# Kernel optimization log

Hardware: AMD Instinct MI355X
Metric: run time of the kernel (lower is better)

## Reference

```python
import jax, jax.numpy as jnp
import numpy as np

VOCAB = 100000
EMBED = 128
BATCH = 65536
NEG = 5


def setup_inputs() -> dict:
    key = jax.random.key(0)
    k1, k2, k3, k4, k5 = jax.random.split(key, 5)
    pos_w = jax.random.randint(k1, (BATCH,), 0, VOCAB)
    pos_v = jax.random.randint(k2, (BATCH,), 0, VOCAB)
    neg_v = jax.random.randint(k3, (BATCH, NEG), 0, VOCAB)
    w_table = jax.random.normal(k4, (VOCAB, EMBED), dtype=jnp.float32) * 0.01
    v_table = jax.random.normal(k5, (VOCAB, EMBED), dtype=jnp.float32) * 0.01
    return {"pos_w": pos_w, "pos_v": pos_v, "neg_v": neg_v,
            "w_table": w_table, "v_table": v_table}


def reference(pos_w, pos_v, neg_v, w_table, v_table):
    # Gathers: [B, E] and [B, K, E]
    w_emb = w_table[pos_w]          # [B, E]
    pos_v_emb = v_table[pos_v]      # [B, E]
    neg_v_emb = v_table[neg_v]      # [B, K, E]

    # Positive score: elementwise dot per row
    score1 = jnp.sum(w_emb * pos_v_emb, axis=1)          # [B]
    score1 = jnp.clip(score1, -10.0, 10.0)
    score1 = jax.nn.log_sigmoid(score1)

    # Negative scores: bmm([B,K,E], [B,E,1]) -> [B,K]
    score2 = jnp.einsum('bke,be->bk', neg_v_emb, w_emb)  # [B, K]
    score2 = jnp.clip(score2, -10.0, 10.0)
    score2 = jax.nn.log_sigmoid(-score2)

    loss = -(jnp.sum(score1) + jnp.sum(score2))
    return loss
```

## Files before the change

kernel.cpp:

```cpp
#include <hip/hip_runtime.h>

#define EMBED 128
#define NEG 5
#define ROWS_PER_BLOCK 16

__device__ __forceinline__ float dot8(float4 w0, float4 w1, float4 a0, float4 a1) {
    float s = w0.x * a0.x;
    s = fmaf(w0.y, a0.y, s);
    s = fmaf(w0.z, a0.z, s);
    s = fmaf(w0.w, a0.w, s);
    s = fmaf(w1.x, a1.x, s);
    s = fmaf(w1.y, a1.y, s);
    s = fmaf(w1.z, a1.z, s);
    s = fmaf(w1.w, a1.w, s);
    return s;
}

__global__ __launch_bounds__(256) void sgneg_kernel(
    const int* __restrict__ pos_w,
    const int* __restrict__ pos_v,
    const int* __restrict__ neg_v,
    const float* __restrict__ w_table,
    const float* __restrict__ v_table,
    float* __restrict__ out,
    int batch)
{
    const int tid = threadIdx.x;
    const int lane16 = tid & 15;
    const int row = tid >> 4;
    const int b = blockIdx.x * ROWS_PER_BLOCK + row;

    __shared__ float scores[6 * ROWS_PER_BLOCK];
    __shared__ float wsum[4];

    float d0 = 0.f, d1 = 0.f, d2 = 0.f, d3 = 0.f, d4 = 0.f, d5 = 0.f;

    if (b < batch) {
        const int iw  = pos_w[b];
        const int ipv = pos_v[b];
        const int in0 = neg_v[b * NEG + 0];
        const int in1 = neg_v[b * NEG + 1];
        const int in2 = neg_v[b * NEG + 2];
        const int in3 = neg_v[b * NEG + 3];
        const int in4 = neg_v[b * NEG + 4];

        const size_t o0 = (size_t)lane16 * 4;
        const size_t o1 = 64 + (size_t)lane16 * 4;

        const float* wr = w_table + (size_t)iw * EMBED;
        const float4 w0 = *reinterpret_cast<const float4*>(wr + o0);
        const float4 w1 = *reinterpret_cast<const float4*>(wr + o1);

        const float* pr = v_table + (size_t)ipv * EMBED;
        const float* r0 = v_table + (size_t)in0 * EMBED;
        const float* r1 = v_table + (size_t)in1 * EMBED;
        const float* r2 = v_table + (size_t)in2 * EMBED;
        const float* r3 = v_table + (size_t)in3 * EMBED;
        const float* r4 = v_table + (size_t)in4 * EMBED;

        const float4 p0 = *reinterpret_cast<const float4*>(pr + o0);
        const float4 p1 = *reinterpret_cast<const float4*>(pr + o1);
        const float4 a0 = *reinterpret_cast<const float4*>(r0 + o0);
        const float4 a1 = *reinterpret_cast<const float4*>(r0 + o1);
        const float4 b0 = *reinterpret_cast<const float4*>(r1 + o0);
        const float4 b1 = *reinterpret_cast<const float4*>(r1 + o1);
        const float4 c0 = *reinterpret_cast<const float4*>(r2 + o0);
        const float4 c1 = *reinterpret_cast<const float4*>(r2 + o1);
        const float4 e0 = *reinterpret_cast<const float4*>(r3 + o0);
        const float4 e1 = *reinterpret_cast<const float4*>(r3 + o1);
        const float4 f0 = *reinterpret_cast<const float4*>(r4 + o0);
        const float4 f1 = *reinterpret_cast<const float4*>(r4 + o1);

        d0 = dot8(w0, w1, p0, p1);
        d1 = dot8(w0, w1, a0, a1);
        d2 = dot8(w0, w1, b0, b1);
        d3 = dot8(w0, w1, c0, c1);
        d4 = dot8(w0, w1, e0, e1);
        d5 = dot8(w0, w1, f0, f1);
    }

    #pragma unroll
    for (int m = 8; m >= 1; m >>= 1) {
        d0 += __shfl_xor(d0, m, 64);
        d1 += __shfl_xor(d1, m, 64);
        d2 += __shfl_xor(d2, m, 64);
        d3 += __shfl_xor(d3, m, 64);
        d4 += __shfl_xor(d4, m, 64);
        d5 += __shfl_xor(d5, m, 64);
    }

    if (lane16 == 0) {
        scores[0 * ROWS_PER_BLOCK + row] = d0;
        scores[1 * ROWS_PER_BLOCK + row] = d1;
        scores[2 * ROWS_PER_BLOCK + row] = d2;
        scores[3 * ROWS_PER_BLOCK + row] = d3;
        scores[4 * ROWS_PER_BLOCK + row] = d4;
        scores[5 * ROWS_PER_BLOCK + row] = d5;
    }
    __syncthreads();

    float t = 0.0f;
    if (tid < 6 * ROWS_PER_BLOCK) {
        const int k = tid >> 4;
        const int r = tid & 15;
        const int gb = blockIdx.x * ROWS_PER_BLOCK + r;
        if (gb < batch) {
            float s = scores[tid];
            s = fminf(10.0f, fmaxf(-10.0f, s));
            const float arg = (k == 0) ? -s : s;
            t = __logf(1.0f + __expf(arg));
        }
    }

    #pragma unroll
    for (int m = 32; m >= 1; m >>= 1) t += __shfl_xor(t, m, 64);
    if ((tid & 63) == 0) wsum[tid >> 6] = t;
    __syncthreads();
    if (tid == 0) atomicAdd(out, wsum[0] + wsum[1] + wsum[2] + wsum[3]);
}

extern "C" void kernel_launch(void* const* d_in, const int* in_sizes, int n_in,
                              void* d_out, int out_size, void* d_ws, size_t ws_size,
                              hipStream_t stream) {
    const int*   pos_w   = (const int*)d_in[0];
    const int*   pos_v   = (const int*)d_in[1];
    const int*   neg_v   = (const int*)d_in[2];
    const float* w_table = (const float*)d_in[3];
    const float* v_table = (const float*)d_in[4];
    float* out = (float*)d_out;

    const int batch = in_sizes[0];

    hipMemsetAsync(out, 0, sizeof(float), stream);

    const int blocks = (batch + ROWS_PER_BLOCK - 1) / ROWS_PER_BLOCK;
    sgneg_kernel<<<blocks, 256, 0, stream>>>(pos_w, pos_v, neg_v,
                                             w_table, v_table, out, batch);
}
```

Measured before the change: 167.1 us.

## Process four rows per 16-lane group to raise memory-level parallelism

Each 16-lane group now handles four batch rows, so a block covers 64 rows. All index loads and 56 float4 gathers are issued before any compute, which raises the number of outstanding memory requests per thread. It also cuts the block count and the number of atomics by a factor of four. The cost is much higher register pressure, which the launch_bounds hint of 4 caps, and out-of-range rows are clamped to the last row instead of skipped.

Result: faster. 141.4 us (-15.4%).

```diff
diff --git a/kernel.cpp b/kernel.cpp
--- a/kernel.cpp
+++ b/kernel.cpp
@@ -2,21 +2,10 @@
 
 #define EMBED 128
 #define NEG 5
-#define ROWS_PER_BLOCK 16
+#define RPG 4
+#define ROWS_PER_BLOCK 64
 
-__device__ __forceinline__ float dot8(float4 w0, float4 w1, float4 a0, float4 a1) {
-    float s = w0.x * a0.x;
-    s = fmaf(w0.y, a0.y, s);
-    s = fmaf(w0.z, a0.z, s);
-    s = fmaf(w0.w, a0.w, s);
-    s = fmaf(w1.x, a1.x, s);
-    s = fmaf(w1.y, a1.y, s);
-    s = fmaf(w1.z, a1.z, s);
-    s = fmaf(w1.w, a1.w, s);
-    return s;
-}
-
-__global__ __launch_bounds__(256) void sgneg_kernel(
+__global__ __launch_bounds__(256, 4) void sgneg_kernel(
     const int* __restrict__ pos_w,
     const int* __restrict__ pos_v,
     const int* __restrict__ neg_v,
@@ -27,88 +16,97 @@
 {
     const int tid = threadIdx.x;
     const int lane16 = tid & 15;
-    const int row = tid >> 4;
-    const int b = blockIdx.x * ROWS_PER_BLOCK + row;
+    const int grp = tid >> 4;
 
     __shared__ float scores[6 * ROWS_PER_BLOCK];
     __shared__ float wsum[4];
 
-    float d0 = 0.f, d1 = 0.f, d2 = 0.f, d3 = 0.f, d4 = 0.f, d5 = 0.f;
+    const size_t o0 = (size_t)lane16 * 4;
+    const size_t o1 = o0 + 64;
 
-    if (b < batch) {
-        const int iw  = pos_w[b];
-        const int ipv = pos_v[b];
-        const int in0 = neg_v[b * NEG + 0];
-        const int in1 = neg_v[b * NEG + 1];
-        const int in2 = neg_v[b * NEG + 2];
-        const int in3 = neg_v[b * NEG + 3];
-        const int in4 = neg_v[b * NEG + 4];
+    int idx[RPG][7];
+    int rowOk[RPG];
+    #pragma unroll
+    for (int r = 0; r < RPG; ++r) {
+        int b = blockIdx.x * ROWS_PER_BLOCK + grp * RPG + r;
+        rowOk[r] = (b < batch);
+        int bc = rowOk[r] ? b : (batch - 1);
+        idx[r][0] = pos_w[bc];
+        idx[r][1] = pos_v[bc];
+        idx[r][2] = neg_v[bc * NEG + 0];
+        idx[r][3] = neg_v[bc * NEG + 1];
+        idx[r][4] = neg_v[bc * NEG + 2];
+        idx[r][5] = neg_v[bc * NEG + 3];
+        idx[r][6] = neg_v[bc * NEG + 4];
+    }
 
-        const size_t o0 = (size_t)lane16 * 4;
-        const size_t o1 = 64 + (size_t)lane16 * 4;
+    float4 lo[RPG][7], hi[RPG][7];
+    #pragma unroll
+    for (int r = 0; r < RPG; ++r) {
+        #pragma unroll
+        for (int j = 0; j < 7; ++j) {
+            const float* base = (j == 0 ? w_table : v_table) + (size_t)idx[r][j] * EMBED;
+            lo[r][j] = *reinterpret_cast<const float4*>(base + o0);
+            hi[r][j] = *reinterpret_cast<const float4*>(base + o1);
+        }
+    }
 
-        const float* wr = w_table + (size_t)iw * EMBED;
-        const float4 w0 = *reinterpret_cast<const float4*>(wr + o0);
-        const float4 w1 = *reinterpret_cast<const float4*>(wr + o1);
-
-        const float* pr = v_table + (size_t)ipv * EMBED;
-        const float* r0 = v_table + (size_t)in0 * EMBED;
-        const float* r1 = v_table + (size_t)in1 * EMBED;
-        const float* r2 = v_table + (size_t)in2 * EMBED;
-        const float* r3 = v_table + (size_t)in3 * EMBED;
-        const float* r4 = v_table + (size_t)in4 * EMBED;
-
-        const float4 p0 = *reinterpret_cast<const float4*>(pr + o0);
-        const float4 p1 = *reinterpret_cast<const float4*>(pr + o1);
-        const float4 a0 = *reinterpret_cast<const float4*>(r0 + o0);
-        const float4 a1 = *reinterpret_cast<const float4*>(r0 + o1);
-        const float4 b0 = *reinterpret_cast<const float4*>(r1 + o0);
-        const float4 b1 = *reinterpret_cast<const float4*>(r1 + o1);
-        const float4 c0 = *reinterpret_cast<const float4*>(r2 + o0);
-        const float4 c1 = *reinterpret_cast<const float4*>(r2 + o1);
-        const float4 e0 = *reinterpret_cast<const float4*>(r3 + o0);
-        const float4 e1 = *reinterpret_cast<const float4*>(r3 + o1);
-        const float4 f0 = *reinterpret_cast<const float4*>(r4 + o0);
-        const float4 f1 = *reinterpret_cast<const float4*>(r4 + o1);
-
-        d0 = dot8(w0, w1, p0, p1);
-        d1 = dot8(w0, w1, a0, a1);
-        d2 = dot8(w0, w1, b0, b1);
-        d3 = dot8(w0, w1, c0, c1);
-        d4 = dot8(w0, w1, e0, e1);
-        d5 = dot8(w0, w1, f0, f1);
+    float d[RPG][6];
+    #pragma unroll
+    for (int r = 0; r < RPG; ++r) {
+        #pragma unroll
+        for (int k = 0; k < 6; ++k) {
+            float4 w0 = lo[r][0], w1 = hi[r][0];
+            float4 a0 = lo[r][k + 1], a1 = hi[r][k + 1];
+            float s = w0.x * a0.x;
+            s = fmaf(w0.y, a0.y, s);
+            s = fmaf(w0.z, a0.z, s);
+            s = fmaf(w0.w, a0.w, s);
+            s = fmaf(w1.x, a1.x, s);
+            s = fmaf(w1.y, a1.y, s);
+            s = fmaf(w1.z, a1.z, s);
+            s = fmaf(w1.w, a1.w, s);
+            d[r][k] = s;
+        }
     }
 
     #pragma unroll
     for (int m = 8; m >= 1; m >>= 1) {
-        d0 += __shfl_xor(d0, m, 64);
-        d1 += __shfl_xor(d1, m, 64);
-        d2 += __shfl_xor(d2, m, 64);
-        d3 += __shfl_xor(d3, m, 64);
-        d4 += __shfl_xor(d4, m, 64);
-        d5 += __shfl_xor(d5, m, 64);
+        #pragma unroll
+        for (int r = 0; r < RPG; ++r) {
+            #pragma unroll
+            for (int k = 0; k < 6; ++k) {
+                d[r][k] += __shfl_xor(d[r][k], m, 64);
+            }
+        }
     }
 
     if (lane16 == 0) {
-        scores[0 * ROWS_PER_BLOCK + row] = d0;
-        scores[1 * ROWS_PER_BLOCK + row] = d1;
-        scores[2 * ROWS_PER_BLOCK + row] = d2;
-        scores[3 * ROWS_PER_BLOCK + row] = d3;
-        scores[4 * ROWS_PER_BLOCK + row] = d4;
-        scores[5 * ROWS_PER_BLOCK + row] = d5;
+        #pragma unroll
+        for (int r = 0; r < RPG; ++r) {
+            const int row = grp * RPG + r;
+            #pragma unroll
+            for (int k = 0; k < 6; ++k) {
+                scores[k * ROWS_PER_BLOCK + row] = d[r][k];
+            }
+        }
     }
     __syncthreads();
 
     float t = 0.0f;
-    if (tid < 6 * ROWS_PER_BLOCK) {
-        const int k = tid >> 4;
-        const int r = tid & 15;
-        const int gb = blockIdx.x * ROWS_PER_BLOCK + r;
-        if (gb < batch) {
-            float s = scores[tid];
-            s = fminf(10.0f, fmaxf(-10.0f, s));
-            const float arg = (k == 0) ? -s : s;
-            t = __logf(1.0f + __expf(arg));
+    #pragma unroll
+    for (int pass = 0; pass < 2; ++pass) {
+        const int i = tid + pass * 256;
+        if (i < 6 * ROWS_PER_BLOCK) {
+            const int k = i / ROWS_PER_BLOCK;
+            const int r = i - k * ROWS_PER_BLOCK;
+            const int gb = blockIdx.x * ROWS_PER_BLOCK + r;
+            if (gb < batch) {
+                float s = scores[i];
+                s = fminf(10.0f, fmaxf(-10.0f, s));
+                const float arg = (k == 0) ? -s : s;
+                t += __logf(1.0f + __expf(arg));
+            }
         }
     }
 
```
